# Performance work log

Hardware: AMD Instinct MI355X
Metric: run time of the kernel (lower is better)

Reference implementation:

```python
import jax, jax.numpy as jnp
import numpy as np

EMB = 64
L = 2
NU = 100000
NI = 50000
ER = 1000000
ET = 800000
EP = 200000


def setup_inputs() -> dict:
    key = jax.random.key(0)
    ks = jax.random.split(key, 32)
    f = jnp.float32
    def nrm(k, shape, s=0.01):
        return (jax.random.normal(k, shape) * s).astype(f)
    inp = {}
    # graph structure (int)
    inp['rate_src'] = jax.random.randint(ks[0], (ER,), 0, NU)
    inp['rate_dst'] = jax.random.randint(ks[1], (ER,), 0, NI)
    inp['trust_src'] = jax.random.randint(ks[2], (ET,), 0, NU)
    inp['trust_dst'] = jax.random.randint(ks[3], (ET,), 0, NU)
    inp['pos_u'] = jax.random.randint(ks[4], (EP,), 0, NU)
    inp['pos_i'] = jax.random.randint(ks[5], (EP,), 0, NI)
    inp['neg_u'] = jax.random.randint(ks[6], (EP,), 0, NU)
    inp['neg_i'] = jax.random.randint(ks[7], (EP,), 0, NI)
    # embeddings (init normal(0, 0.01) per init_weights)
    inp['eu'] = nrm(ks[8], (NU, EMB))
    inp['ei'] = nrm(ks[9], (NI, EMB))
    # per-rel GATv2 params, stacked over L layers; [:,0]=fc_src, [:,1]=fc_dst
    inp['rate_W'] = nrm(ks[10], (L, 2, EMB, EMB))
    inp['rate_b'] = jnp.zeros((L, 2, EMB), f)
    inp['rate_attn'] = nrm(ks[11], (L, EMB), 0.1)
    inp['rate_bias'] = jnp.zeros((L, EMB), f)
    inp['rb_W'] = nrm(ks[12], (L, 2, EMB, EMB))
    inp['rb_b'] = jnp.zeros((L, 2, EMB), f)
    inp['rb_attn'] = nrm(ks[13], (L, EMB), 0.1)
    inp['rb_bias'] = jnp.zeros((L, EMB), f)
    inp['tr_W'] = nrm(ks[14], (L, 2, EMB, EMB))
    inp['tr_b'] = jnp.zeros((L, 2, EMB), f)
    inp['tr_attn'] = nrm(ks[15], (L, EMB), 0.1)
    inp['tr_bias'] = jnp.zeros((L, EMB), f)
    # attention-gate MLPs: [:, 0]=influence, [:, 1]=interest
    inp['attW1'] = nrm(ks[16], (L, 2, 2 * EMB, 2 * EMB))
    inp['attb1'] = jnp.zeros((L, 2, 2 * EMB), f)
    inp['attW2'] = nrm(ks[17], (L, 2, 2 * EMB))
    inp['attb2'] = jnp.zeros((L, 2), f)
    return inp


def gatv2(hs, hd, src, dst, Ws, bs, Wd, bd, attn, bias, n_dst):
    # DGL GATv2Conv, num_heads=1: e = attn . leaky_relu(Ws h_u + Wd h_v), slope 0.2
    fs = hs @ Ws + bs          # [Ns, E]
    fd = hd @ Wd + bd          # [Nd, E]
    e = jax.nn.leaky_relu(fs[src] + fd[dst], 0.2) @ attn  # [E]
    m = jax.ops.segment_max(e, dst, num_segments=n_dst)
    ex = jnp.exp(e - m[dst])
    denom = jax.ops.segment_sum(ex, dst, num_segments=n_dst)
    alpha = ex / denom[dst]
    out = jax.ops.segment_sum(alpha[:, None] * fs[src], dst, num_segments=n_dst)
    return out + bias


def _bn1(x):
    # BatchNorm1d(1), training-mode batch stats, affine identity at init
    mu = jnp.mean(x)
    var = jnp.mean((x - mu) ** 2)
    return (x - mu) * jax.lax.rsqrt(var + 1e-5)


def reference(eu, ei, rate_W, rate_b, rate_attn, rate_bias, rb_W, rb_b, rb_attn,
              rb_bias, tr_W, tr_b, tr_attn, tr_bias, attW1, attb1, attW2, attb2,
              rate_src, rate_dst, trust_src, trust_dst, pos_u, pos_i, neg_u, neg_i):
    n_users, n_items = eu.shape[0], ei.shape[0]
    hu, hi = eu, ei
    res_u, res_i = [eu], [ei]
    for l in range(rate_W.shape[0]):
        # interest diffusion: rate (user->item) and rated-by (item->user, reverse edges)
        hi_new = gatv2(hu, hi, rate_src, rate_dst, rate_W[l, 0], rate_b[l, 0],
                       rate_W[l, 1], rate_b[l, 1], rate_attn[l], rate_bias[l], n_items) + hi
        q = gatv2(hi, hu, rate_dst, rate_src, rb_W[l, 0], rb_b[l, 0],
                  rb_W[l, 1], rb_b[l, 1], rb_attn[l], rb_bias[l], n_users)
        # influence diffusion: trust (user->user)
        p = gatv2(hu, hu, trust_src, trust_dst, tr_W[l, 0], tr_b[l, 0],
                  tr_W[l, 1], tr_b[l, 1], tr_attn[l], tr_bias[l], n_users)
        def att(h2, i):
            z = (h2 @ attW1[l, i] + attb1[l, i]) @ attW2[l, i] + attb2[l, i]  # [N]
            return jax.nn.leaky_relu(_bn1(z), 0.01)
        a_inf = att(jnp.concatenate([hu, p], axis=1), 0)
        a_int = att(jnp.concatenate([hu, q], axis=1), 1)
        gamma = jax.nn.softmax(jnp.stack([a_inf, a_int], axis=1), axis=1)  # [N,2]
        hu = gamma[:, 0:1] * p + gamma[:, 1:2] * q + hu
        hi = hi_new
        res_u.append(hu)
        res_i.append(hi)
    hu_all = jnp.concatenate(res_u, axis=1)  # [NU, EMB*(1+L)]
    hi_all = jnp.concatenate(res_i, axis=1)
    pos = jnp.sum(hu_all[pos_u] * hi_all[pos_i], axis=1, keepdims=True)  # [EP,1]
    neg = jnp.sum(hu_all[neg_u] * hi_all[neg_i], axis=1, keepdims=True)
    return pos, neg
```

## Files before the change

### kernel.cpp

```cpp
#include <hip/hip_runtime.h>
#include <hip/hip_bf16.h>
#include <hip/hip_fp16.h>
#include <cstdint>

typedef __hip_bfloat16 bf16;
typedef __attribute__((ext_vector_type(8))) short frag_ab;
typedef __attribute__((ext_vector_type(4))) float frag_cd;
typedef __attribute__((ext_vector_type(4))) short short4v;
typedef __attribute__((ext_vector_type(8))) short short8v;
typedef unsigned short u16;

#define CAPA 56
#define CAPB 40
#define CAPC 32

__device__ __forceinline__ float b2f(short s){
  return __uint_as_float(((unsigned)(unsigned short)s) << 16);
}
__device__ __forceinline__ float h2f(short s){
  __half h; __builtin_memcpy(&h, &s, 2); return __half2float(h);
}
__device__ __forceinline__ short f2h_s(float x){
  __half h = __float2half(x);
  short s; __builtin_memcpy(&s, &h, 2); return s;
}
__device__ __forceinline__ void bf_split(float x, short& hi, short& lo){
  bf16 h = __float2bfloat16(x);
  float hf = __bfloat162float(h);
  bf16 l = __float2bfloat16(x - hf);
  __builtin_memcpy(&hi, &h, 2);
  __builtin_memcpy(&lo, &l, 2);
}

__device__ __forceinline__ float wave_sum(float v){
#pragma unroll
  for (int o = 32; o > 0; o >>= 1) v += __shfl_down(v, o, 64);
  return v;
}

__global__ void k_wsplit(const float* __restrict__ rateW, const float* __restrict__ rbW,
                         const float* __restrict__ trW,
                         short* __restrict__ Whi, short* __restrict__ Wlo){
  int tid = blockIdx.x * 256 + threadIdx.x;
  if (tid >= 12 * 4096) return;
  int m = tid >> 12, rem = tid & 4095;
  int lane = rem >> 6, rem2 = rem & 63;
  int pair = rem2 >> 3, j = rem2 & 7;
  int c = pair >> 1, h = pair & 1;
  int rel = m >> 2, li = m & 3;
  const float* base = (rel == 0) ? rateW : (rel == 1) ? rbW : trW;
  float v = base[(size_t)li * 4096 + (32 * h + (lane >> 4) * 8 + j) * 64 + 16 * c + (lane & 15)];
  short sh, sl; bf_split(v, sh, sl);
  Whi[tid] = sh; Wlo[tid] = sl;
}

__device__ __forceinline__ void dev_linear(int rowb, int nloc, int gofs, int nglob,
    const float* __restrict__ x, int xs, int xo,
    const short* __restrict__ Whi, const short* __restrict__ Wlo, int mcount,
    int m0, int m1, int m2, int m3,
    const float* b0, const float* b1, const float* b2, const float* b3,
    bf16* o0, bf16* o1, bf16* o2, bf16* o3){
  int lane = threadIdx.x & 63, w = threadIdx.x >> 6;
  int quad = lane >> 4, n16 = lane & 15;
  int rowbase = rowb + w * 16;
  if (rowbase >= nloc) return;
  int lrow = rowbase + n16; if (lrow >= nloc) lrow = nloc - 1;
  const float* xp = x + (size_t)lrow * xs + xo;
  frag_ab ahi[2], alo[2];
#pragma unroll
  for (int h = 0; h < 2; ++h){
    frag_ab vh, vl;
#pragma unroll
    for (int j = 0; j < 8; ++j){
      float xv = xp[32 * h + quad * 8 + j];
      short sh, sl; bf_split(xv, sh, sl);
      vh[j] = sh; vl[j] = sl;
    }
    ahi[h] = vh; alo[h] = vl;
  }
  int ms[4] = {m0, m1, m2, m3};
  const float* bs[4] = {b0, b1, b2, b3};
  bf16* os[4] = {o0, o1, o2, o3};
  for (int i = 0; i < mcount; ++i){
    const frag_ab* Bh = (const frag_ab*)(Whi + (size_t)ms[i] * 4096 + lane * 64);
    const frag_ab* Bl = (const frag_ab*)(Wlo + (size_t)ms[i] * 4096 + lane * 64);
    frag_cd acc[4];
#pragma unroll
    for (int c = 0; c < 4; ++c) acc[c] = frag_cd{0.f, 0.f, 0.f, 0.f};
#pragma unroll
    for (int c = 0; c < 4; ++c)
#pragma unroll
      for (int h = 0; h < 2; ++h){
        frag_ab bh = Bh[c * 2 + h], bl = Bl[c * 2 + h];
        acc[c] = __builtin_amdgcn_mfma_f32_16x16x32_bf16(ahi[h], bh, acc[c], 0, 0, 0);
        acc[c] = __builtin_amdgcn_mfma_f32_16x16x32_bf16(alo[h], bh, acc[c], 0, 0, 0);
        acc[c] = __builtin_amdgcn_mfma_f32_16x16x32_bf16(ahi[h], bl, acc[c], 0, 0, 0);
      }
    const float* bb = bs[i];
    bf16* oo = os[i];
#pragma unroll
    for (int reg = 0; reg < 4; ++reg){
      int r = rowbase + quad * 4 + reg;
      if (r >= nloc || gofs + r >= nglob) continue;
#pragma unroll
      for (int c = 0; c < 4; ++c)
        oo[(size_t)(gofs + r) * 64 + 16 * c + n16] = __float2bfloat16(acc[c][reg] + bb[16 * c + n16]);
    }
  }
}

struct LinArgs {
  int nblk; const float* x; int xs, xo, n, mcount;
  int m0, m1, m2, m3;
  const float *b0, *b1, *b2, *b3;
  bf16 *o0, *o1, *o2, *o3;
};
struct PrepArgs {
  int NBH, NBC, ER, ET, NU, NI;
  const int *rate_src, *rate_dst, *trust_dst;
  int *cntA, *cntB, *cntC;
  u16 *posA, *posB, *posC;
  const float *eu, *ei;
  float *hu01, *hi01;
  const short *Whi, *Wlo;
  LinArgs LU, LI;
  const float *W1, *b1v, *W2, *b2v;
  float *vvec, *cs;
};

__global__ void k_prep(PrepArgs a){
  int b = blockIdx.x, t = threadIdx.x;
  if (b < a.NBH){
    int k = b * 256 + t;
    if (k < a.ER){
      int d = a.rate_dst[k], s = a.rate_src[k];
      a.posA[k] = (u16)atomicAdd(a.cntA + d, 1);
      a.posB[k] = (u16)atomicAdd(a.cntB + s, 1);
    }
    if (k < a.ET){
      a.posC[k] = (u16)atomicAdd(a.cntC + a.trust_dst[k], 1);
    }
    return;
  }
  b -= a.NBH;
  if (b < a.LU.nblk){
    dev_linear(b * 64, a.LU.n, 0, a.LU.n, a.LU.x, a.LU.xs, a.LU.xo, a.Whi, a.Wlo,
               a.LU.mcount, a.LU.m0, a.LU.m1, a.LU.m2, a.LU.m3,
               a.LU.b0, a.LU.b1, a.LU.b2, a.LU.b3, a.LU.o0, a.LU.o1, a.LU.o2, a.LU.o3);
    return;
  }
  b -= a.LU.nblk;
  if (b < a.LI.nblk){
    dev_linear(b * 64, a.LI.n, 0, a.LI.n, a.LI.x, a.LI.xs, a.LI.xo, a.Whi, a.Wlo,
               a.LI.mcount, a.LI.m0, a.LI.m1, a.LI.m2, a.LI.m3,
               a.LI.b0, a.LI.b1, a.LI.b2, a.LI.b3, a.LI.o0, a.LI.o1, a.LI.o2, a.LI.o3);
    return;
  }
  b -= a.LI.nblk;
  if (b < a.NBC){
    int tot = (a.NU + a.NI) * 16;
    int tu = a.NU * 16;
    int base = b * 1024 + t;
#pragma unroll
    for (int s = 0; s < 4; ++s){
      int idx = base + s * 256;
      if (idx >= tot) break;
      if (idx < tu){
        int r = idx >> 4, jj = idx & 15;
        *(float4*)(a.hu01 + (size_t)r * 128 + 4 * jj) =
            *(const float4*)(a.eu + (size_t)r * 64 + 4 * jj);
      } else {
        int t2 = idx - tu;
        int r = t2 >> 4, jj = t2 & 15;
        *(float4*)(a.hi01 + (size_t)r * 128 + 4 * jj) =
            *(const float4*)(a.ei + (size_t)r * 64 + 4 * jj);
      }
    }
    return;
  }
  for (int it = t; it < 512; it += 256){
    int li = it >> 7, r = it & 127;
    float acc = 0.f;
    for (int c = 0; c < 128; ++c)
      acc += a.W1[(size_t)(li * 128 + r) * 128 + c] * a.W2[li * 128 + c];
    a.vvec[li * 128 + r] = acc;
    if (r == 0){
      float cacc = a.b2v[li];
      for (int c = 0; c < 128; ++c)
        cacc += a.b1v[li * 128 + c] * a.W2[li * 128 + c];
      a.cs[li] = cacc;
    }
  }
}

__global__ void k_fill(const int* __restrict__ rs_, const int* __restrict__ rd_,
                       const int* __restrict__ ts_, const int* __restrict__ td_,
                       const u16* __restrict__ posA, const u16* __restrict__ posB,
                       const u16* __restrict__ posC,
                       int* __restrict__ csrA, u16* __restrict__ csrB,
                       int* __restrict__ csrC, int ER, int ET){
  int k = blockIdx.x * 256 + threadIdx.x;
  if (k < ER){
    int s = rs_[k], d = rd_[k];
    int pa = posA[k], pb = posB[k];
    if (pa < CAPA) csrA[(size_t)d * CAPA + pa] = s;
    if (pb < CAPB) csrB[(size_t)s * CAPB + pb] = (u16)d;
  }
  if (k < ET){
    int pc = posC[k];
    if (pc < CAPC) csrC[(size_t)td_[k] * CAPC + pc] = ts_[k];
  }
}

struct GatArgs {
  int nblk, n, cap, of16;
  const int *cnt;
  const int *csr; const u16 *csr16;
  const bf16 *fs, *fd;
  const float *attn, *bias;
  void *out; int os, oo;
  const float *res; int rs, ro;
};

__device__ __forceinline__ void dev_gat(int lb, const GatArgs& g){
  int d = lb * 4 + (threadIdx.x >> 6);
  if (d >= g.n) return;
  int lane = threadIdx.x & 63;
  int gg = lane >> 3, l8 = lane & 7;
  int c = g.cnt[d]; if (c > g.cap) c = g.cap;
  size_t base = (size_t)d * g.cap;
  int my_s = 0;
  if (lane < c) my_s = g.csr16 ? (int)g.csr16[base + lane] : g.csr[base + lane];
  short8v dv = *(const short8v*)(g.fd + (size_t)d * 64 + 8 * l8);
  float fdv[8];
#pragma unroll
  for (int j = 0; j < 8; ++j) fdv[j] = b2f(dv[j]);
  float4 a0 = *(const float4*)(g.attn + 8 * l8);
  float4 a1 = *(const float4*)(g.attn + 8 * l8 + 4);
  float a8[8] = {a0.x, a0.y, a0.z, a0.w, a1.x, a1.y, a1.z, a1.w};
  float acc[8];
#pragma unroll
  for (int j = 0; j < 8; ++j) acc[j] = 0.f;
  float den = 0.f;
  int s_cur = __shfl(my_s, gg, 64);
  short8v sv = *(const short8v*)(g.fs + (size_t)s_cur * 64 + 8 * l8);
  for (int idx = 0; idx < c; idx += 8){
    short8v svn = sv;
    int nn = idx + 8;
    if (nn < c){
      int s_nxt = __shfl(my_s, nn + gg, 64);
      svn = *(const short8v*)(g.fs + (size_t)s_nxt * 64 + 8 * l8);
    }
    bool valid = (idx + gg) < c;
    float f[8];
    float tt = 0.f;
#pragma unroll
    for (int j = 0; j < 8; ++j){
      f[j] = b2f(sv[j]);
      float v = f[j] + fdv[j];
      v = (v > 0.f) ? v : 0.2f * v;
      tt += v * a8[j];
    }
#pragma unroll
    for (int o = 1; o < 8; o <<= 1) tt += __shfl_xor(tt, o, 64);
    float ex = valid ? __expf(tt) : 0.f;
#pragma unroll
    for (int j = 0; j < 8; ++j) acc[j] += ex * f[j];
    den += ex;
    sv = svn;
  }
#pragma unroll
  for (int o = 8; o < 64; o <<= 1){
#pragma unroll
    for (int j = 0; j < 8; ++j) acc[j] += __shfl_xor(acc[j], o, 64);
    den += __shfl_xor(den, o, 64);
  }
  if (gg == 0){
    float inv = (den > 0.f) ? 1.f / den : 0.f;
    float4 b0 = *(const float4*)(g.bias + 8 * l8);
    float4 b1 = *(const float4*)(g.bias + 8 * l8 + 4);
    float o8[8];
    o8[0] = acc[0] * inv + b0.x; o8[1] = acc[1] * inv + b0.y;
    o8[2] = acc[2] * inv + b0.z; o8[3] = acc[3] * inv + b0.w;
    o8[4] = acc[4] * inv + b1.x; o8[5] = acc[5] * inv + b1.y;
    o8[6] = acc[6] * inv + b1.z; o8[7] = acc[7] * inv + b1.w;
    if (g.res){
      float4 r0 = *(const float4*)(g.res + (size_t)d * g.rs + g.ro + 8 * l8);
      float4 r1 = *(const float4*)(g.res + (size_t)d * g.rs + g.ro + 8 * l8 + 4);
      o8[0] += r0.x; o8[1] += r0.y; o8[2] += r0.z; o8[3] += r0.w;
      o8[4] += r1.x; o8[5] += r1.y; o8[6] += r1.z; o8[7] += r1.w;
    }
    if (g.of16){
      short8v hv;
#pragma unroll
      for (int j = 0; j < 8; ++j) hv[j] = f2h_s(o8[j]);
      *(short8v*)((short*)g.out + (size_t)d * g.os + g.oo + 8 * l8) = hv;
    } else {
      float* op = (float*)g.out + (size_t)d * g.os + g.oo + 8 * l8;
      *(float4*)op = make_float4(o8[0], o8[1], o8[2], o8[3]);
      *(float4*)(op + 4) = make_float4(o8[4], o8[5], o8[6], o8[7]);
    }
  }
}

__global__ void k_gat3(GatArgs A, GatArgs B, GatArgs C){
  int b = blockIdx.x;
  if (b < A.nblk){ dev_gat(b, A); return; }
  b -= A.nblk;
  if (b < B.nblk){ dev_gat(b, B); return; }
  b -= B.nblk;
  dev_gat(b, C);
}

struct GzArgs {
  int nbz, NU, l;
  const float* hu01;
  const __half* pf16;
  const __half* q;
  const float *vvec, *cs;
  float *z1, *z2, *bsums;
  const short *Whi, *Wlo;
  LinArgs LI;
};

__global__ void k_gatez(GzArgs a){
  int b = blockIdx.x;
  if (b >= a.nbz){
    int blk = b - a.nbz;
    dev_linear(blk * 64, a.LI.n, 0, a.LI.n, a.LI.x, a.LI.xs, a.LI.xo, a.Whi, a.Wlo,
               a.LI.mcount, a.LI.m0, a.LI.m1, a.LI.m2, a.LI.m3,
               a.LI.b0, a.LI.b1, a.LI.b2, a.LI.b3, a.LI.o0, a.LI.o1, a.LI.o2, a.LI.o3);
    return;
  }
  __shared__ float part[4][4];
  int w = threadIdx.x >> 6, j = threadIdx.x & 63;
  int nidx = b * 4 + w;
  float lz1 = 0.f, lz2 = 0.f;
  if (nidx < a.NU){
    const float* v1 = a.vvec + a.l * 256;
    const float* v2 = a.vvec + a.l * 256 + 128;
    float h  = a.hu01[(size_t)nidx * 128 + a.l * 64 + j];
    float pv = a.pf16 ? h2f(((const short*)a.pf16)[(size_t)nidx * 64 + j])
                      : a.hu01[(size_t)nidx * 128 + 64 + j];
    float qv = h2f(((const short*)a.q)[(size_t)nidx * 64 + j]);
    float t1 = wave_sum(h * v1[j] + pv * v1[64 + j]);
    float t2 = wave_sum(h * v2[j] + qv * v2[64 + j]);
    if (j == 0){
      lz1 = t1 + a.cs[a.l * 2 + 0];
      lz2 = t2 + a.cs[a.l * 2 + 1];
      a.z1[nidx] = lz1;
      a.z2[nidx] = lz2;
    }
  }
  if (j == 0){
    part[w][0] = lz1; part[w][1] = lz1 * lz1;
    part[w][2] = lz2; part[w][3] = lz2 * lz2;
  }
  __syncthreads();
  if (threadIdx.x < 4)
    a.bsums[(size_t)b * 4 + threadIdx.x] =
        part[0][threadIdx.x] + part[1][threadIdx.x] +
        part[2][threadIdx.x] + part[3][threadIdx.x];
}

__global__ void k_bn(const float* __restrict__ bsums, int nb,
                     double* __restrict__ gpart, double* __restrict__ sums,
                     int* __restrict__ tick){
  __shared__ double sh[256];
  __shared__ int lastflag;
  int c = threadIdx.x & 3, r0 = blockIdx.x * 64 + (threadIdx.x >> 2);
  double acc = 0.0;
  for (int i = r0; i < nb; i += gridDim.x * 64)
    acc += (double)bsums[(size_t)i * 4 + c];
  sh[threadIdx.x] = acc;
  __syncthreads();
  for (int s = 128; s >= 4; s >>= 1){
    if (threadIdx.x < s) sh[threadIdx.x] += sh[threadIdx.x + s];
    __syncthreads();
  }
  if (threadIdx.x < 4) gpart[(size_t)blockIdx.x * 4 + threadIdx.x] = sh[threadIdx.x];
  __threadfence();
  if (threadIdx.x == 0) lastflag = (atomicAdd(tick, 1) == (int)gridDim.x - 1);
  __syncthreads();
  if (lastflag){
    __threadfence();
    int k0 = threadIdx.x >> 2;
    double a2 = 0.0;
    for (int i = k0; i < (int)gridDim.x; i += 64) a2 += gpart[(size_t)i * 4 + c];
    sh[threadIdx.x] = a2;
    __syncthreads();
    for (int s = 128; s >= 4; s >>= 1){
      if (threadIdx.x < s) sh[threadIdx.x] += sh[threadIdx.x + s];
      __syncthreads();
    }
    if (threadIdx.x < 4) sums[threadIdx.x] = sh[threadIdx.x];
  }
}

struct CmbArgs {
  int l, NU;
  float* hu01; __half* hu2; const __half* q;
  const float *z1, *z2; const double* sums;
  int dolin;
  const short *Whi, *Wlo;
  int m0, m1, m2, m3;
  const float *b0, *b1, *b2, *b3;
  bf16 *o0, *o1, *o2, *o3;
};

__global__ void k_combine(CmbArgs a){
  __shared__ float lds[64][65];
  int r0 = blockIdx.x * 64;
  int t = threadIdx.x;
  double invn = 1.0 / (double)a.NU;
  double mu1 = a.sums[0] * invn, mu2 = a.sums[2] * invn;
  float var1 = (float)(a.sums[1] * invn - mu1 * mu1);
  float var2 = (float)(a.sums[3] * invn - mu2 * mu2);
  float rs1 = rsqrtf(var1 + 1e-5f), rs2 = rsqrtf(var2 + 1e-5f);
  int nloc = a.NU - r0; if (nloc > 64) nloc = 64;
#pragma unroll
  for (int s = 0; s < 16; ++s){
    int elem = s * 256 + t;
    int row = elem >> 6, col = elem & 63;
    if (row < nloc){
      int r = r0 + row;
      float a1 = (a.z1[r] - (float)mu1) * rs1;
      float a2 = (a.z2[r] - (float)mu2) * rs2;
      a1 = a1 > 0.f ? a1 : 0.01f * a1;
      a2 = a2 > 0.f ? a2 : 0.01f * a2;
      float mx = fmaxf(a1, a2);
      float e1 = __expf(a1 - mx), e2 = __expf(a2 - mx);
      float inv = 1.f / (e1 + e2);
      float pv = (a.l == 0) ? a.hu01[(size_t)r * 128 + 64 + col]
                            : h2f(((const short*)a.hu2)[(size_t)r * 64 + col]);
      float qv = h2f(((const short*)a.q)[(size_t)r * 64 + col]);
      float h  = a.hu01[(size_t)r * 128 + a.l * 64 + col];
      float out = e1 * inv * pv + e2 * inv * qv + h;
      if (a.l == 0){
        a.hu01[(size_t)r * 128 + 64 + col] = out;
        lds[row][col] = out;
      } else {
        ((short*)a.hu2)[(size_t)r * 64 + col] = f2h_s(out);
      }
    }
  }
  if (!a.dolin) return;
  __syncthreads();
  dev_linear(0, nloc, r0, a.NU, &lds[0][0], 65, 0, a.Whi, a.Wlo, 4,
             a.m0, a.m1, a.m2, a.m3, a.b0, a.b1, a.b2, a.b3,
             a.o0, a.o1, a.o2, a.o3);
}

__global__ void k_score(const int* __restrict__ pu, const int* __restrict__ pi,
                        const int* __restrict__ nu, const int* __restrict__ ni,
                        const float* __restrict__ hu01, const __half* __restrict__ hu2,
                        const float* __restrict__ hi01, const __half* __restrict__ hi2,
                        float* __restrict__ out, int EP){
  int gw = blockIdx.x * 4 + (threadIdx.x >> 6);
  int sub = (threadIdx.x >> 4) & 3, l16 = threadIdx.x & 15;
  int k = gw * 4 + sub;
  if (k >= 2 * EP) return;
  int u, i;
  if (k < EP){ u = pu[k]; i = pi[k]; } else { u = nu[k - EP]; i = ni[k - EP]; }
  const float4* A = (const float4*)(hu01 + (size_t)u * 128);
  const float4* B = (const float4*)(hi01 + (size_t)i * 128);
  float acc = 0.f;
#pragma unroll
  for (int t = 0; t < 2; ++t){
    float4 av = A[l16 + 16 * t];
    float4 bv = B[l16 + 16 * t];
    acc += av.x * bv.x + av.y * bv.y + av.z * bv.z + av.w * bv.w;
  }
  short4v ha = *(const short4v*)((const short*)hu2 + (size_t)u * 64 + 4 * l16);
  short4v hb = *(const short4v*)((const short*)hi2 + (size_t)i * 64 + 4 * l16);
  acc += h2f(ha[0]) * h2f(hb[0]) + h2f(ha[1]) * h2f(hb[1])
       + h2f(ha[2]) * h2f(hb[2]) + h2f(ha[3]) * h2f(hb[3]);
#pragma unroll
  for (int o = 8; o > 0; o >>= 1) acc += __shfl_xor(acc, o, 64);
  if (l16 == 0) out[k] = acc;
}

extern "C" void kernel_launch(void* const* d_in, const int* in_sizes, int n_in,
                              void* d_out, int out_size, void* d_ws, size_t ws_size,
                              hipStream_t stream) {
  const int*   rate_src  = (const int*)  d_in[0];
  const int*   rate_dst  = (const int*)  d_in[1];
  const int*   trust_src = (const int*)  d_in[2];
  const int*   trust_dst = (const int*)  d_in[3];
  const int*   pos_u     = (const int*)  d_in[4];
  const int*   pos_i     = (const int*)  d_in[5];
  const int*   neg_u     = (const int*)  d_in[6];
  const int*   neg_i     = (const int*)  d_in[7];
  const float* eu        = (const float*)d_in[8];
  const float* ei        = (const float*)d_in[9];
  const float* rate_W    = (const float*)d_in[10];
  const float* rate_b    = (const float*)d_in[11];
  const float* rate_attn = (const float*)d_in[12];
  const float* rate_bias = (const float*)d_in[13];
  const float* rb_W      = (const float*)d_in[14];
  const float* rb_b      = (const float*)d_in[15];
  const float* rb_attn   = (const float*)d_in[16];
  const float* rb_bias   = (const float*)d_in[17];
  const float* tr_W      = (const float*)d_in[18];
  const float* tr_b      = (const float*)d_in[19];
  const float* tr_attn   = (const float*)d_in[20];
  const float* tr_bias   = (const float*)d_in[21];
  const float* attW1     = (const float*)d_in[22];
  const float* attb1     = (const float*)d_in[23];
  const float* attW2     = (const float*)d_in[24];
  const float* attb2     = (const float*)d_in[25];

  const int ER = in_sizes[0];
  const int ET = in_sizes[2];
  const int EP = in_sizes[4];
  const int NU = in_sizes[8] / 64;
  const int NI = in_sizes[9] / 64;
  const int EM = (ER > ET) ? ER : ET;

  float*  wsp    = (float*)d_ws;
  float*  hu01   = wsp;
  float*  hi01   = hu01 + (size_t)NU * 128;
  __half* hi2    = (__half*)(hi01 + (size_t)NI * 128);
  __half* hu2    = hi2 + (size_t)NI * 64;
  __half* qf     = hu2 + (size_t)NU * 64;
  u16*    posA   = (u16*)qf;
  u16*    posB   = posA + ER;
  u16*    posC   = posB + ER;
  bf16*   fdA    = (bf16*)(qf + (size_t)NU * 64);
  bf16*   fsB    = fdA + (size_t)NI * 64;
  bf16*   tb     = fsB + (size_t)NI * 64;
  bf16*   fsA    = tb;
  bf16*   fdB    = tb + (size_t)NU * 64;
  bf16*   fsC    = tb + (size_t)NU * 128;
  bf16*   fdC    = tb + (size_t)NU * 192;
  float*  z1     = (float*)(tb + (size_t)NU * 256);
  float*  z2     = z1 + NU;
  float*  bsums  = z2 + NU;
  float*  vvec   = bsums + (size_t)(((NU + 3) / 4) * 4);
  float*  cs     = vvec + 512;
  double* sums   = (double*)(((uintptr_t)(cs + 4) + 15) & ~(uintptr_t)15);
  double* gpart  = sums + 4;
  short*  Whi    = (short*)(gpart + 512);
  short*  Wlo    = Whi + 12 * 4096;
  int*    cntA   = (int*)(Wlo + 12 * 4096);
  int*    cntB   = cntA + NI;
  int*    cntC   = cntB + NU;
  int*    tick   = cntC + NU;
  int*    csrA   = tick + 8;
  u16*    csrB   = (u16*)(csrA + (size_t)NI * CAPA);
  int*    csrC   = (int*)(csrB + (size_t)NU * CAPB);

  auto cdiv = [](int a, int b){ return (a + b - 1) / b; };
  const int nbz = cdiv(NU, 4);

  hipMemsetAsync(cntA, 0, (size_t)(NI + 2 * NU + 8) * 4, stream);
  k_wsplit<<<192, 256, 0, stream>>>(rate_W, rb_W, tr_W, Whi, Wlo);

  PrepArgs pa;
  pa.NBH = cdiv(EM, 256);
  pa.NBC = cdiv((NU + NI) * 16, 1024);
  pa.ER = ER; pa.ET = ET; pa.NU = NU; pa.NI = NI;
  pa.rate_src = rate_src; pa.rate_dst = rate_dst; pa.trust_dst = trust_dst;
  pa.cntA = cntA; pa.cntB = cntB; pa.cntC = cntC;
  pa.posA = posA; pa.posB = posB; pa.posC = posC;
  pa.eu = eu; pa.ei = ei; pa.hu01 = hu01; pa.hi01 = hi01;
  pa.Whi = Whi; pa.Wlo = Wlo;
  pa.LU.nblk = cdiv(NU, 64); pa.LU.x = eu; pa.LU.xs = 64; pa.LU.xo = 0;
  pa.LU.n = NU; pa.LU.mcount = 4;
  pa.LU.m0 = 0; pa.LU.m1 = 5; pa.LU.m2 = 8; pa.LU.m3 = 9;
  pa.LU.b0 = rate_b + 0;  pa.LU.b1 = rb_b + 64;
  pa.LU.b2 = tr_b + 0;    pa.LU.b3 = tr_b + 64;
  pa.LU.o0 = fsA; pa.LU.o1 = fdB; pa.LU.o2 = fsC; pa.LU.o3 = fdC;
  pa.LI.nblk = cdiv(NI, 64); pa.LI.x = ei; pa.LI.xs = 64; pa.LI.xo = 0;
  pa.LI.n = NI; pa.LI.mcount = 2;
  pa.LI.m0 = 1; pa.LI.m1 = 4; pa.LI.m2 = 0; pa.LI.m3 = 0;
  pa.LI.b0 = rate_b + 64; pa.LI.b1 = rb_b + 0;
  pa.LI.b2 = nullptr; pa.LI.b3 = nullptr;
  pa.LI.o0 = fdA; pa.LI.o1 = fsB; pa.LI.o2 = nullptr; pa.LI.o3 = nullptr;
  pa.W1 = attW1; pa.b1v = attb1; pa.W2 = attW2; pa.b2v = attb2;
  pa.vvec = vvec; pa.cs = cs;
  k_prep<<<pa.NBH + pa.LU.nblk + pa.LI.nblk + pa.NBC + 1, 256, 0, stream>>>(pa);

  k_fill<<<cdiv(EM, 256), 256, 0, stream>>>(rate_src, rate_dst, trust_src, trust_dst,
      posA, posB, posC, csrA, csrB, csrC, ER, ET);

  for (int l = 0; l < 2; ++l){
    GatArgs A, B, C;
    A.nblk = cdiv(NI, 4); A.n = NI; A.cap = CAPA;
    A.cnt = cntA; A.csr = csrA; A.csr16 = nullptr; A.fs = fsA; A.fd = fdA;
    A.attn = rate_attn + l * 64; A.bias = rate_bias + l * 64;
    if (l == 0){ A.of16 = 0; A.out = hi01; A.os = 128; A.oo = 64;
                 A.res = hi01; A.rs = 128; A.ro = 0; }
    else       { A.of16 = 1; A.out = hi2;  A.os = 64;  A.oo = 0;
                 A.res = hi01; A.rs = 128; A.ro = 64; }
    B.nblk = cdiv(NU, 4); B.n = NU; B.cap = CAPB; B.of16 = 1;
    B.cnt = cntB; B.csr = nullptr; B.csr16 = csrB; B.fs = fsB; B.fd = fdB;
    B.attn = rb_attn + l * 64; B.bias = rb_bias + l * 64;
    B.out = qf; B.os = 64; B.oo = 0;
    B.res = nullptr; B.rs = 0; B.ro = 0;
    C.nblk = cdiv(NU, 4); C.n = NU; C.cap = CAPC;
    C.cnt = cntC; C.csr = csrC; C.csr16 = nullptr; C.fs = fsC; C.fd = fdC;
    C.attn = tr_attn + l * 64; C.bias = tr_bias + l * 64;
    if (l == 0){ C.of16 = 0; C.out = hu01; C.os = 128; C.oo = 64; }
    else       { C.of16 = 1; C.out = hu2;  C.os = 64;  C.oo = 0;  }
    C.res = nullptr; C.rs = 0; C.ro = 0;
    k_gat3<<<A.nblk + B.nblk + C.nblk, 256, 0, stream>>>(A, B, C);

    GzArgs gz;
    gz.nbz = nbz; gz.NU = NU; gz.l = l;
    gz.hu01 = hu01; gz.pf16 = (l == 0) ? nullptr : hu2; gz.q = qf;
    gz.vvec = vvec; gz.cs = cs; gz.z1 = z1; gz.z2 = z2; gz.bsums = bsums;
    gz.Whi = Whi; gz.Wlo = Wlo;
    if (l == 0){
      gz.LI.nblk = cdiv(NI, 64); gz.LI.x = hi01; gz.LI.xs = 128; gz.LI.xo = 64;
      gz.LI.n = NI; gz.LI.mcount = 2;
      gz.LI.m0 = 3; gz.LI.m1 = 6; gz.LI.m2 = 0; gz.LI.m3 = 0;
      gz.LI.b0 = rate_b + 192; gz.LI.b1 = rb_b + 128;
      gz.LI.b2 = nullptr; gz.LI.b3 = nullptr;
      gz.LI.o0 = fdA; gz.LI.o1 = fsB; gz.LI.o2 = nullptr; gz.LI.o3 = nullptr;
    } else {
      gz.LI.nblk = 0; gz.LI.x = nullptr; gz.LI.xs = 0; gz.LI.xo = 0;
      gz.LI.n = 0; gz.LI.mcount = 0;
      gz.LI.m0 = gz.LI.m1 = gz.LI.m2 = gz.LI.m3 = 0;
      gz.LI.b0 = gz.LI.b1 = gz.LI.b2 = gz.LI.b3 = nullptr;
      gz.LI.o0 = gz.LI.o1 = gz.LI.o2 = gz.LI.o3 = nullptr;
    }
    k_gatez<<<nbz + gz.LI.nblk, 256, 0, stream>>>(gz);

    k_bn<<<128, 256, 0, stream>>>(bsums, nbz, gpart, sums, tick + l);

    CmbArgs cm;
    cm.l = l; cm.NU = NU;
    cm.hu01 = hu01; cm.hu2 = hu2; cm.q = qf;
    cm.z1 = z1; cm.z2 = z2; cm.sums = sums;
    cm.dolin = (l == 0) ? 1 : 0;
    cm.Whi = Whi; cm.Wlo = Wlo;
    cm.m0 = 2; cm.m1 = 7; cm.m2 = 10; cm.m3 = 11;
    cm.b0 = rate_b + 128; cm.b1 = rb_b + 192;
    cm.b2 = tr_b + 128;   cm.b3 = tr_b + 192;
    cm.o0 = fsA; cm.o1 = fdB; cm.o2 = fsC; cm.o3 = fdC;
    k_combine<<<cdiv(NU, 64), 256, 0, stream>>>(cm);
  }

  k_score<<<cdiv(2 * EP, 16), 256, 0, stream>>>(pos_u, pos_i, neg_u, neg_i,
      hu01, hu2, hi01, hi2, (float*)d_out, EP);
}
```

Before: 882.4 us.

## Add packed fp16 score buffers and rebalance prep/fill kernel work

Writes a packed fp16 copy of all three layer embeddings (192 halves per row) for users and items as they are produced. The final scoring then uses one contiguous half-precision gather per row instead of mixed fp32/fp16 buffers, with 8 pairs per wave. It also moves the initial linear projections from the prep kernel into the CSR fill kernel and interleaves histogram/fill blocks with other work by proportional block index mapping. The trade-offs are extra fp16 writes and workspace, and lower precision in the layer-0/1 embeddings used for scoring.

```diff
diff --git a/kernel.cpp b/kernel.cpp
--- a/kernel.cpp
+++ b/kernel.cpp
@@ -115,23 +115,25 @@
   const float *b0, *b1, *b2, *b3;
   bf16 *o0, *o1, *o2, *o3;
 };
+
 struct PrepArgs {
-  int NBH, NBC, ER, ET, NU, NI;
+  int NBH, NBC, TOT, ER, ET, NU, NI;
   const int *rate_src, *rate_dst, *trust_dst;
   int *cntA, *cntB, *cntC;
   u16 *posA, *posB, *posC;
   const float *eu, *ei;
   float *hu01, *hi01;
-  const short *Whi, *Wlo;
-  LinArgs LU, LI;
+  __half *huF, *hiF;
   const float *W1, *b1v, *W2, *b2v;
   float *vvec, *cs;
 };
 
 __global__ void k_prep(PrepArgs a){
-  int b = blockIdx.x, t = threadIdx.x;
-  if (b < a.NBH){
-    int k = b * 256 + t;
+  int bid = blockIdx.x, t = threadIdx.x;
+  long long hb = ((long long)bid * a.NBH) / a.TOT;
+  bool ishist = (((long long)(bid + 1) * a.NBH) / a.TOT) > hb;
+  if (ishist){
+    int k = (int)hb * 256 + t;
     if (k < a.ER){
       int d = a.rate_dst[k], s = a.rate_src[k];
       a.posA[k] = (u16)atomicAdd(a.cntA + d, 1);
@@ -142,38 +144,34 @@
     }
     return;
   }
-  b -= a.NBH;
-  if (b < a.LU.nblk){
-    dev_linear(b * 64, a.LU.n, 0, a.LU.n, a.LU.x, a.LU.xs, a.LU.xo, a.Whi, a.Wlo,
-               a.LU.mcount, a.LU.m0, a.LU.m1, a.LU.m2, a.LU.m3,
-               a.LU.b0, a.LU.b1, a.LU.b2, a.LU.b3, a.LU.o0, a.LU.o1, a.LU.o2, a.LU.o3);
-    return;
-  }
-  b -= a.LU.nblk;
-  if (b < a.LI.nblk){
-    dev_linear(b * 64, a.LI.n, 0, a.LI.n, a.LI.x, a.LI.xs, a.LI.xo, a.Whi, a.Wlo,
-               a.LI.mcount, a.LI.m0, a.LI.m1, a.LI.m2, a.LI.m3,
-               a.LI.b0, a.LI.b1, a.LI.b2, a.LI.b3, a.LI.o0, a.LI.o1, a.LI.o2, a.LI.o3);
-    return;
-  }
-  b -= a.LI.nblk;
-  if (b < a.NBC){
+  int sb = bid - (int)hb;
+  if (sb < a.NBC){
     int tot = (a.NU + a.NI) * 16;
     int tu = a.NU * 16;
-    int base = b * 1024 + t;
+    int base = sb * 1024 + t;
 #pragma unroll
     for (int s = 0; s < 4; ++s){
       int idx = base + s * 256;
       if (idx >= tot) break;
       if (idx < tu){
         int r = idx >> 4, jj = idx & 15;
-        *(float4*)(a.hu01 + (size_t)r * 128 + 4 * jj) =
-            *(const float4*)(a.eu + (size_t)r * 64 + 4 * jj);
+        float4 v = *(const float4*)(a.eu + (size_t)r * 64 + 4 * jj);
+        *(float4*)(a.hu01 + (size_t)r * 128 + 4 * jj) = v;
+        if (a.huF){
+          short4v h;
+          h[0] = f2h_s(v.x); h[1] = f2h_s(v.y); h[2] = f2h_s(v.z); h[3] = f2h_s(v.w);
+          *(short4v*)((short*)a.huF + (size_t)r * 192 + 4 * jj) = h;
+        }
       } else {
         int t2 = idx - tu;
         int r = t2 >> 4, jj = t2 & 15;
-        *(float4*)(a.hi01 + (size_t)r * 128 + 4 * jj) =
-            *(const float4*)(a.ei + (size_t)r * 64 + 4 * jj);
+        float4 v = *(const float4*)(a.ei + (size_t)r * 64 + 4 * jj);
+        *(float4*)(a.hi01 + (size_t)r * 128 + 4 * jj) = v;
+        if (a.hiF){
+          short4v h;
+          h[0] = f2h_s(v.x); h[1] = f2h_s(v.y); h[2] = f2h_s(v.z); h[3] = f2h_s(v.w);
+          *(short4v*)((short*)a.hiF + (size_t)r * 192 + 4 * jj) = h;
+        }
       }
     }
     return;
@@ -193,23 +191,44 @@
   }
 }
 
-__global__ void k_fill(const int* __restrict__ rs_, const int* __restrict__ rd_,
-                       const int* __restrict__ ts_, const int* __restrict__ td_,
-                       const u16* __restrict__ posA, const u16* __restrict__ posB,
-                       const u16* __restrict__ posC,
-                       int* __restrict__ csrA, u16* __restrict__ csrB,
-                       int* __restrict__ csrC, int ER, int ET){
-  int k = blockIdx.x * 256 + threadIdx.x;
-  if (k < ER){
-    int s = rs_[k], d = rd_[k];
-    int pa = posA[k], pb = posB[k];
-    if (pa < CAPA) csrA[(size_t)d * CAPA + pa] = s;
-    if (pb < CAPB) csrB[(size_t)s * CAPB + pb] = (u16)d;
-  }
-  if (k < ET){
-    int pc = posC[k];
-    if (pc < CAPC) csrC[(size_t)td_[k] * CAPC + pc] = ts_[k];
-  }
+struct FillArgs {
+  int NBF, TOT, ER, ET;
+  const int *rs_, *rd_, *ts_, *td_;
+  const u16 *posA, *posB, *posC;
+  int *csrA; u16 *csrB; int *csrC;
+  const short *Whi, *Wlo;
+  LinArgs LU, LI;
+};
+
+__global__ void k_fill(FillArgs a){
+  int bid = blockIdx.x, t = threadIdx.x;
+  long long fb = ((long long)bid * a.NBF) / a.TOT;
+  bool isf = (((long long)(bid + 1) * a.NBF) / a.TOT) > fb;
+  if (isf){
+    int k = (int)fb * 256 + t;
+    if (k < a.ER){
+      int s = a.rs_[k], d = a.rd_[k];
+      int pa = a.posA[k], pb = a.posB[k];
+      if (pa < CAPA) a.csrA[(size_t)d * CAPA + pa] = s;
+      if (pb < CAPB) a.csrB[(size_t)s * CAPB + pb] = (u16)d;
+    }
+    if (k < a.ET){
+      int pc = a.posC[k];
+      if (pc < CAPC) a.csrC[(size_t)a.td_[k] * CAPC + pc] = a.ts_[k];
+    }
+    return;
+  }
+  int sb = bid - (int)fb;
+  if (sb < a.LU.nblk){
+    dev_linear(sb * 64, a.LU.n, 0, a.LU.n, a.LU.x, a.LU.xs, a.LU.xo, a.Whi, a.Wlo,
+               a.LU.mcount, a.LU.m0, a.LU.m1, a.LU.m2, a.LU.m3,
+               a.LU.b0, a.LU.b1, a.LU.b2, a.LU.b3, a.LU.o0, a.LU.o1, a.LU.o2, a.LU.o3);
+    return;
+  }
+  sb -= a.LU.nblk;
+  dev_linear(sb * 64, a.LI.n, 0, a.LI.n, a.LI.x, a.LI.xs, a.LI.xo, a.Whi, a.Wlo,
+             a.LI.mcount, a.LI.m0, a.LI.m1, a.LI.m2, a.LI.m3,
+             a.LI.b0, a.LI.b1, a.LI.b2, a.LI.b3, a.LI.o0, a.LI.o1, a.LI.o2, a.LI.o3);
 }
 
 struct GatArgs {
@@ -220,6 +239,7 @@
   const float *attn, *bias;
   void *out; int os, oo;
   const float *res; int rs, ro;
+  __half *fmir; int mo;
 };
 
 __device__ __forceinline__ void dev_gat(int lb, const GatArgs& g){
@@ -300,6 +320,12 @@
       *(float4*)op = make_float4(o8[0], o8[1], o8[2], o8[3]);
       *(float4*)(op + 4) = make_float4(o8[4], o8[5], o8[6], o8[7]);
     }
+    if (g.fmir){
+      short8v hv;
+#pragma unroll
+      for (int j = 0; j < 8; ++j) hv[j] = f2h_s(o8[j]);
+      *(short8v*)((short*)g.fmir + (size_t)d * 192 + g.mo + 8 * l8) = hv;
+    }
   }
 }
 
@@ -325,13 +351,13 @@
 
 __global__ void k_gatez(GzArgs a){
   int b = blockIdx.x;
-  if (b >= a.nbz){
-    int blk = b - a.nbz;
-    dev_linear(blk * 64, a.LI.n, 0, a.LI.n, a.LI.x, a.LI.xs, a.LI.xo, a.Whi, a.Wlo,
+  if (b < a.LI.nblk){
+    dev_linear(b * 64, a.LI.n, 0, a.LI.n, a.LI.x, a.LI.xs, a.LI.xo, a.Whi, a.Wlo,
                a.LI.mcount, a.LI.m0, a.LI.m1, a.LI.m2, a.LI.m3,
                a.LI.b0, a.LI.b1, a.LI.b2, a.LI.b3, a.LI.o0, a.LI.o1, a.LI.o2, a.LI.o3);
     return;
   }
+  b -= a.LI.nblk;
   __shared__ float part[4][4];
   int w = threadIdx.x >> 6, j = threadIdx.x & 63;
   int nidx = b * 4 + w;
@@ -398,8 +424,9 @@
 }
 
 struct CmbArgs {
-  int l, NU;
+  int l, NU, wh2;
   float* hu01; __half* hu2; const __half* q;
+  __half* fout; int fo_off;
   const float *z1, *z2; const double* sums;
   int dolin;
   const short *Whi, *Wlo;
@@ -439,9 +466,11 @@
       if (a.l == 0){
         a.hu01[(size_t)r * 128 + 64 + col] = out;
         lds[row][col] = out;
-      } else {
+      } else if (a.wh2){
         ((short*)a.hu2)[(size_t)r * 64 + col] = f2h_s(out);
       }
+      if (a.fout)
+        ((short*)a.fout)[(size_t)r * 192 + a.fo_off + col] = f2h_s(out);
     }
   }
   if (!a.dolin) return;
@@ -449,6 +478,31 @@
   dev_linear(0, nloc, r0, a.NU, &lds[0][0], 65, 0, a.Whi, a.Wlo, 4,
              a.m0, a.m1, a.m2, a.m3, a.b0, a.b1, a.b2, a.b3,
              a.o0, a.o1, a.o2, a.o3);
+}
+
+__global__ void k_score_f16(const int* __restrict__ pu, const int* __restrict__ pi,
+                            const int* __restrict__ nu, const int* __restrict__ ni,
+                            const __half* __restrict__ huF, const __half* __restrict__ hiF,
+                            float* __restrict__ out, int EP){
+  int wv = threadIdx.x >> 6, lane = threadIdx.x & 63;
+  int g = lane >> 3, l8 = lane & 7;
+  int k = (blockIdx.x * 4 + wv) * 8 + g;
+  if (k >= 2 * EP) return;
+  int u, i;
+  if (k < EP){ u = pu[k]; i = pi[k]; } else { u = nu[k - EP]; i = ni[k - EP]; }
+  const short8v* A = (const short8v*)((const short*)huF + (size_t)u * 192);
+  const short8v* B = (const short8v*)((const short*)hiF + (size_t)i * 192);
+  float acc = 0.f;
+#pragma unroll
+  for (int t = 0; t < 3; ++t){
+    short8v a = A[l8 + 8 * t];
+    short8v b = B[l8 + 8 * t];
+#pragma unroll
+    for (int j = 0; j < 8; ++j) acc += h2f(a[j]) * h2f(b[j]);
+  }
+#pragma unroll
+  for (int o = 1; o < 8; o <<= 1) acc += __shfl_xor(acc, o, 64);
+  if (l8 == 0) out[k] = acc;
 }
 
 __global__ void k_score(const int* __restrict__ pu, const int* __restrict__ pi,
@@ -549,6 +603,11 @@
   int*    csrA   = tick + 8;
   u16*    csrB   = (u16*)(csrA + (size_t)NI * CAPA);
   int*    csrC   = (int*)(csrB + (size_t)NU * CAPB);
+  uintptr_t fEnd = ((uintptr_t)(csrC + (size_t)NU * CAPC) + 15) & ~(uintptr_t)15;
+  __half* huF = (__half*)fEnd;
+  __half* hiF = huF + (size_t)NU * 192;
+  size_t need = (uintptr_t)(hiF + (size_t)NI * 192) - (uintptr_t)d_ws;
+  bool ft = (need <= ws_size);
 
   auto cdiv = [](int a, int b){ return (a + b - 1) / b; };
   const int nbz = cdiv(NU, 4);
@@ -559,51 +618,66 @@
   PrepArgs pa;
   pa.NBH = cdiv(EM, 256);
   pa.NBC = cdiv((NU + NI) * 16, 1024);
+  pa.TOT = pa.NBH + pa.NBC + 1;
   pa.ER = ER; pa.ET = ET; pa.NU = NU; pa.NI = NI;
   pa.rate_src = rate_src; pa.rate_dst = rate_dst; pa.trust_dst = trust_dst;
   pa.cntA = cntA; pa.cntB = cntB; pa.cntC = cntC;
   pa.posA = posA; pa.posB = posB; pa.posC = posC;
   pa.eu = eu; pa.ei = ei; pa.hu01 = hu01; pa.hi01 = hi01;
-  pa.Whi = Whi; pa.Wlo = Wlo;
-  pa.LU.nblk = cdiv(NU, 64); pa.LU.x = eu; pa.LU.xs = 64; pa.LU.xo = 0;
-  pa.LU.n = NU; pa.LU.mcount = 4;
-  pa.LU.m0 = 0; pa.LU.m1 = 5; pa.LU.m2 = 8; pa.LU.m3 = 9;
-  pa.LU.b0 = rate_b + 0;  pa.LU.b1 = rb_b + 64;
-  pa.LU.b2 = tr_b + 0;    pa.LU.b3 = tr_b + 64;
-  pa.LU.o0 = fsA; pa.LU.o1 = fdB; pa.LU.o2 = fsC; pa.LU.o3 = fdC;
-  pa.LI.nblk = cdiv(NI, 64); pa.LI.x = ei; pa.LI.xs = 64; pa.LI.xo = 0;
-  pa.LI.n = NI; pa.LI.mcount = 2;
-  pa.LI.m0 = 1; pa.LI.m1 = 4; pa.LI.m2 = 0; pa.LI.m3 = 0;
-  pa.LI.b0 = rate_b + 64; pa.LI.b1 = rb_b + 0;
-  pa.LI.b2 = nullptr; pa.LI.b3 = nullptr;
-  pa.LI.o0 = fdA; pa.LI.o1 = fsB; pa.LI.o2 = nullptr; pa.LI.o3 = nullptr;
+  pa.huF = ft ? huF : (__half*)nullptr;
+  pa.hiF = ft ? hiF : (__half*)nullptr;
   pa.W1 = attW1; pa.b1v = attb1; pa.W2 = attW2; pa.b2v = attb2;
   pa.vvec = vvec; pa.cs = cs;
-  k_prep<<<pa.NBH + pa.LU.nblk + pa.LI.nblk + pa.NBC + 1, 256, 0, stream>>>(pa);
-
-  k_fill<<<cdiv(EM, 256), 256, 0, stream>>>(rate_src, rate_dst, trust_src, trust_dst,
-      posA, posB, posC, csrA, csrB, csrC, ER, ET);
+  k_prep<<<pa.TOT, 256, 0, stream>>>(pa);
+
+  FillArgs fa;
+  fa.NBF = cdiv(EM, 256);
+  fa.ER = ER; fa.ET = ET;
+  fa.rs_ = rate_src; fa.rd_ = rate_dst; fa.ts_ = trust_src; fa.td_ = trust_dst;
+  fa.posA = posA; fa.posB = posB; fa.posC = posC;
+  fa.csrA = csrA; fa.csrB = csrB; fa.csrC = csrC;
+  fa.Whi = Whi; fa.Wlo = Wlo;
+  fa.LU.nblk = cdiv(NU, 64); fa.LU.x = eu; fa.LU.xs = 64; fa.LU.xo = 0;
+  fa.LU.n = NU; fa.LU.mcount = 4;
+  fa.LU.m0 = 0; fa.LU.m1 = 5; fa.LU.m2 = 8; fa.LU.m3 = 9;
+  fa.LU.b0 = rate_b + 0;  fa.LU.b1 = rb_b + 64;
+  fa.LU.b2 = tr_b + 0;    fa.LU.b3 = tr_b + 64;
+  fa.LU.o0 = fsA; fa.LU.o1 = fdB; fa.LU.o2 = fsC; fa.LU.o3 = fdC;
+  fa.LI.nblk = cdiv(NI, 64); fa.LI.x = ei; fa.LI.xs = 64; fa.LI.xo = 0;
+  fa.LI.n = NI; fa.LI.mcount = 2;
+  fa.LI.m0 = 1; fa.LI.m1 = 4; fa.LI.m2 = 0; fa.LI.m3 = 0;
+  fa.LI.b0 = rate_b + 64; fa.LI.b1 = rb_b + 0;
+  fa.LI.b2 = nullptr; fa.LI.b3 = nullptr;
+  fa.LI.o0 = fdA; fa.LI.o1 = fsB; fa.LI.o2 = nullptr; fa.LI.o3 = nullptr;
+  fa.TOT = fa.NBF + fa.LU.nblk + fa.LI.nblk;
+  k_fill<<<fa.TOT, 256, 0, stream>>>(fa);
 
   for (int l = 0; l < 2; ++l){
     GatArgs A, B, C;
     A.nblk = cdiv(NI, 4); A.n = NI; A.cap = CAPA;
     A.cnt = cntA; A.csr = csrA; A.csr16 = nullptr; A.fs = fsA; A.fd = fdA;
     A.attn = rate_attn + l * 64; A.bias = rate_bias + l * 64;
-    if (l == 0){ A.of16 = 0; A.out = hi01; A.os = 128; A.oo = 64;
-                 A.res = hi01; A.rs = 128; A.ro = 0; }
-    else       { A.of16 = 1; A.out = hi2;  A.os = 64;  A.oo = 0;
-                 A.res = hi01; A.rs = 128; A.ro = 64; }
+    A.fmir = nullptr; A.mo = 0;
+    if (l == 0){
+      A.of16 = 0; A.out = hi01; A.os = 128; A.oo = 64;
+      A.res = hi01; A.rs = 128; A.ro = 0;
+      if (ft){ A.fmir = hiF; A.mo = 64; }
+    } else {
+      A.res = hi01; A.rs = 128; A.ro = 64;
+      if (ft){ A.of16 = 1; A.out = hiF; A.os = 192; A.oo = 128; }
+      else   { A.of16 = 1; A.out = hi2;  A.os = 64;  A.oo = 0;  }
+    }
     B.nblk = cdiv(NU, 4); B.n = NU; B.cap = CAPB; B.of16 = 1;
     B.cnt = cntB; B.csr = nullptr; B.csr16 = csrB; B.fs = fsB; B.fd = fdB;
     B.attn = rb_attn + l * 64; B.bias = rb_bias + l * 64;
     B.out = qf; B.os = 64; B.oo = 0;
-    B.res = nullptr; B.rs = 0; B.ro = 0;
+    B.res = nullptr; B.rs = 0; B.ro = 0; B.fmir = nullptr; B.mo = 0;
     C.nblk = cdiv(NU, 4); C.n = NU; C.cap = CAPC;
     C.cnt = cntC; C.csr = csrC; C.csr16 = nullptr; C.fs = fsC; C.fd = fdC;
     C.attn = tr_attn + l * 64; C.bias = tr_bias + l * 64;
+    C.res = nullptr; C.rs = 0; C.ro = 0; C.fmir = nullptr; C.mo = 0;
     if (l == 0){ C.of16 = 0; C.out = hu01; C.os = 128; C.oo = 64; }
     else       { C.of16 = 1; C.out = hu2;  C.os = 64;  C.oo = 0;  }
-    C.res = nullptr; C.rs = 0; C.ro = 0;
     k_gat3<<<A.nblk + B.nblk + C.nblk, 256, 0, stream>>>(A, B, C);
 
     GzArgs gz;
@@ -633,6 +707,9 @@
     cm.l = l; cm.NU = NU;
     cm.hu01 = hu01; cm.hu2 = hu2; cm.q = qf;
     cm.z1 = z1; cm.z2 = z2; cm.sums = sums;
+    cm.wh2 = (l == 1 && !ft) ? 1 : 0;
+    cm.fout = ft ? huF : (__half*)nullptr;
+    cm.fo_off = (l == 0) ? 64 : 128;
     cm.dolin = (l == 0) ? 1 : 0;
     cm.Whi = Whi; cm.Wlo = Wlo;
     cm.m0 = 2; cm.m1 = 7; cm.m2 = 10; cm.m3 = 11;
@@ -642,6 +719,10 @@
     k_combine<<<cdiv(NU, 64), 256, 0, stream>>>(cm);
   }
 
-  k_score<<<cdiv(2 * EP, 16), 256, 0, stream>>>(pos_u, pos_i, neg_u, neg_i,
-      hu01, hu2, hi01, hi2, (float*)d_out, EP);
-}
+  if (ft)
+    k_score_f16<<<cdiv(2 * EP, 32), 256, 0, stream>>>(pos_u, pos_i, neg_u, neg_i,
+        huF, hiF, (float*)d_out, EP);
+  else
+    k_score<<<cdiv(2 * EP, 16), 256, 0, stream>>>(pos_u, pos_i, neg_u, neg_i,
+        hu01, hu2, hi01, hi2, (float*)d_out, EP);
+}
```

Measured after the change: 960.1 us. +8.8%, slower.
